# Optimization experiments

Hardware: AMD Instinct MI355X
Metric: run time of the kernel (lower is better)

The kernel has to match this reference:

```python
import jax, jax.numpy as jnp
import numpy as np

BIG_NUMBER = 1000000.0
B, N, H = 8, 256, 128   # batch, nodes, node/hidden feat
E, G = 128, 128         # edge feat, graph feat
MID, OUT = 128, 128
IN_Z = 2 * H


def setup_inputs() -> dict:
    key = jax.random.key(0)
    ks = jax.random.split(key, 20)
    sc = lambda fan_in: 1.0 / np.sqrt(fan_in)
    inp = {
        "node_fts": jax.random.normal(ks[0], (B, N, H), jnp.float32),
        "edge_fts": jax.random.normal(ks[1], (B, N, N, E), jnp.float32),
        "graph_fts": jax.random.normal(ks[2], (B, G), jnp.float32),
        "adj_mat": (jax.random.uniform(ks[3], (B, N, N)) < 0.5).astype(jnp.float32),
        "hidden": jax.random.normal(ks[4], (B, N, H), jnp.float32),
        # linear params, stored [in, out]
        "W1": jax.random.normal(ks[5], (IN_Z, MID), jnp.float32) * sc(IN_Z),
        "b1": jnp.zeros((MID,), jnp.float32),
        "W2": jax.random.normal(ks[6], (IN_Z, MID), jnp.float32) * sc(IN_Z),
        "b2": jnp.zeros((MID,), jnp.float32),
        "We": jax.random.normal(ks[7], (E, MID), jnp.float32) * sc(E),
        "be": jnp.zeros((MID,), jnp.float32),
        "Wg": jax.random.normal(ks[8], (G, MID), jnp.float32) * sc(G),
        "bg": jnp.zeros((MID,), jnp.float32),
        "Wo1": jax.random.normal(ks[9], (IN_Z, OUT), jnp.float32) * sc(IN_Z),
        "bo1": jnp.zeros((OUT,), jnp.float32),
        "Wo2": jax.random.normal(ks[10], (MID, OUT), jnp.float32) * sc(MID),
        "bo2": jnp.zeros((OUT,), jnp.float32),
    }
    return inp


def reference(node_fts, edge_fts, graph_fts, adj_mat, hidden,
              W1, b1, W2, b2, We, be, Wg, bg, Wo1, bo1, Wo2, bo2):
    # z: [b, n, 2h]
    z = jnp.concatenate([node_fts, hidden], axis=-1)
    msg_1 = z @ W1 + b1                       # [b, n, mid]
    msg_2 = z @ W2 + b2                       # [b, n, mid]
    msg_e = edge_fts @ We + be                # [b, n, n, mid]
    msg_g = graph_fts @ Wg + bg               # [b, mid]
    # msgs[b, i, j, :]; reduce over i (senders)
    msgs = (msg_1[:, None, :, :] + msg_2[:, :, None, :]
            + msg_e + msg_g[:, None, None, :])
    maxarg = jnp.where(adj_mat[..., None] > 0, msgs, -BIG_NUMBER)
    msgs_red = jnp.max(maxarg, axis=1)        # [b, n, mid]
    ret = jax.nn.relu((z @ Wo1 + bo1) + (msgs_red @ Wo2 + bo2))
    return ret
```

## Files before the change

kernel.cpp:

```cpp
#include <hip/hip_runtime.h>
#include <hip/hip_bf16.h>
#include <stdint.h>
#include <stddef.h>

#define B_   8
#define N_   256
#define H_   128
#define E_   128
#define INZ  256
#define BIGN 1000000.0f

typedef float f32x4 __attribute__((ext_vector_type(4)));
typedef short bf16x8 __attribute__((ext_vector_type(8)));

static __device__ __forceinline__ unsigned cvt2(float a, float b) {
    unsigned short ra = __builtin_bit_cast(unsigned short, __float2bfloat16(a));
    unsigned short rb = __builtin_bit_cast(unsigned short, __float2bfloat16(b));
    return (unsigned)ra | ((unsigned)rb << 16);
}

static __device__ __forceinline__ bf16x8 mk_frag(f32x4 lo, f32x4 h4) {
    union { unsigned u[4]; bf16x8 v; } r;
    r.u[0] = cvt2(lo.x, lo.y);
    r.u[1] = cvt2(lo.z, lo.w);
    r.u[2] = cvt2(h4.x, h4.y);
    r.u[3] = cvt2(h4.z, h4.w);
    return r.v;
}

#define GL16(gp, lp) __builtin_amdgcn_global_load_lds(                        \
    (const __attribute__((address_space(1))) unsigned int*)(gp),              \
    (__attribute__((address_space(3))) unsigned int*)(lp), 16, 0, 0)

__global__ __launch_bounds__(256) void prep_kernel(
    const float* __restrict__ node, const float* __restrict__ hidden,
    const float* __restrict__ gf,
    const float* __restrict__ W1, const float* __restrict__ b1,
    const float* __restrict__ W2, const float* __restrict__ b2,
    const float* __restrict__ Wg, const float* __restrict__ bg,
    const float* __restrict__ Wo1, const float* __restrict__ bo1,
    const float* __restrict__ We,
    float* __restrict__ msg1, float* __restrict__ m2g,
    float* __restrict__ zo1, unsigned short* __restrict__ weT)
{
    __shared__ float zs[4][INZ];
    const int t  = threadIdx.x;
    const int r0 = blockIdx.x * 4;
    const int b  = r0 >> 8;

    for (int idx = t; idx < 4 * INZ; idx += 256) {
        int r = idx >> 8, k = idx & 255;
        int row = r0 + r;
        zs[r][k] = (k < H_) ? node[(size_t)row * H_ + k]
                            : hidden[(size_t)row * H_ + (k - H_)];
    }
    if (blockIdx.x < 8) {
        int e0 = blockIdx.x * 2048;
        for (int e = e0 + t; e < e0 + 2048; e += 256) {
            int n = e >> 7, k = e & 127;
            weT[(n * 128 + k) ^ ((n & 7) << 3)] =
                (unsigned short)__builtin_bit_cast(unsigned short,
                    __float2bfloat16(We[k * 128 + n]));
        }
    }
    __syncthreads();

    const int col = t & 127;
    const int rg  = t >> 7;
    float a1[2] = {0, 0}, a2[2] = {0, 0}, ao[2] = {0, 0};

#pragma unroll 4
    for (int k = 0; k < INZ; ++k) {
        float w1 = W1[k * 128 + col];
        float w2 = W2[k * 128 + col];
        float wo = Wo1[k * 128 + col];
#pragma unroll
        for (int rr = 0; rr < 2; ++rr) {
            float zv = zs[rg * 2 + rr][k];
            a1[rr] = fmaf(zv, w1, a1[rr]);
            a2[rr] = fmaf(zv, w2, a2[rr]);
            ao[rr] = fmaf(zv, wo, ao[rr]);
        }
    }
    float mg = bg[col];
#pragma unroll 4
    for (int g = 0; g < 128; ++g)
        mg = fmaf(gf[b * 128 + g], Wg[g * 128 + col], mg);

    const float bb1 = b1[col], bb2 = b2[col], bbo = bo1[col];
#pragma unroll
    for (int rr = 0; rr < 2; ++rr) {
        size_t row = (size_t)(r0 + rg * 2 + rr);
        msg1[row * 128 + col] = a1[rr] + bb1;
        m2g[row * 128 + col]  = a2[rr] + bb2 + mg;
        zo1[row * 128 + col]  = ao[rr] + bbo;
    }
}

__global__ __launch_bounds__(256, 3) void pgn_main(
    const float* __restrict__ edge, const float* __restrict__ adj,
    const float* __restrict__ m2g, const unsigned short* __restrict__ weT,
    float* __restrict__ redp, int nsplit)
{
    __shared__ __align__(16) char smem[49152];

    const int t    = threadIdx.x;
    const int lane = t & 63, wid = t >> 6;
    const int wr   = wid >> 1, wn = wid & 1;
    const int hi   = lane >> 4, c15 = lane & 15;
    const int blk  = blockIdx.x;
    const int ih   = blk % nsplit;
    const int jblk = blk / nsplit;
    const int b    = jblk >> 6, jt = jblk & 63;
    const int j0   = jt * 4;
    const int irange = N_ / nsplit;
    const int ibase  = ih * irange;
    const int nt     = irange >> 3;

    bf16x8 bfr[4][4];
#pragma unroll
    for (int n = 0; n < 4; ++n) {
        int col = wn * 64 + n * 16 + c15;
        int sw  = (col & 7) << 3;
#pragma unroll
        for (int ks = 0; ks < 4; ++ks) {
            int sidx = (col * 128 + ks * 32 + hi * 8) ^ sw;
            bfr[n][ks] = *(const bf16x8*)(weT + sidx);
        }
    }

    const int l2 = lane >> 5;
    const int wb = (lane & 31) * 16;
    const char* gq0; const char* gq1; const char* gq2; const char* gq3;
    {
        const char* eb = (const char*)edge;
#pragma unroll
        for (int q = 0; q < 4; ++q) {
            int tr = wid * 8 + 2 * q + l2;
            int il = tr >> 2, jj = tr & 3;
            int sb = wb ^ ((tr & 7) << 4);
            const char* g = eb +
                (((size_t)(b * N_) + ibase + il) * N_ + (j0 + jj)) * 512 + sb;
            if (q == 0) gq0 = g; else if (q == 1) gq1 = g;
            else if (q == 2) gq2 = g; else gq3 = g;
        }
    }
    const unsigned woff = (unsigned)__builtin_amdgcn_readfirstlane(wid * 4096);

    char* pa = smem;
    char* pb = smem + 16384;
    char* pc = smem + 32768;

    GL16(gq0, pa + woff);
    GL16(gq1, pa + woff + 1024);
    GL16(gq2, pa + woff + 2048);
    GL16(gq3, pa + woff + 3072);

    const int trc = wr * 16 + c15;
    const unsigned abase = (unsigned)((trc * 512 + hi * 32) ^ ((trc & 7) << 4));
    const int il_l = wr * 4 + hi;

    float rmax[4][4];
#pragma unroll
    for (int n = 0; n < 4; ++n)
#pragma unroll
        for (int rg = 0; rg < 4; ++rg) rmax[n][rg] = -BIGN;

    for (int it = 0; it < nt; ++it) {
        const int ig = ibase + it * 8 + il_l;
        f32x4 a4 = *(const f32x4*)(adj + (size_t)(b * N_ + ig) * N_ + j0);
        const float* mp = m2g + (size_t)(b * N_ + ig) * 128 + wn * 64 + c15;
        float mv0 = mp[0], mv1 = mp[16], mv2 = mp[32], mv3 = mp[48];

        if (it + 1 < nt) {
            size_t toff = (size_t)(it + 1) * (8u * N_ * E_ * 4u);
            GL16(gq0 + toff, pb + woff);
            GL16(gq1 + toff, pb + woff + 1024);
            GL16(gq2 + toff, pb + woff + 2048);
            GL16(gq3 + toff, pb + woff + 3072);
            asm volatile("s_waitcnt vmcnt(9)" ::: "memory");
        } else {
            asm volatile("s_waitcnt vmcnt(5)" ::: "memory");
        }
        __builtin_amdgcn_s_barrier();
        __builtin_amdgcn_sched_barrier(0);

        f32x4 acc[4] = {};
#pragma unroll
        for (int ks = 0; ks < 4; ++ks) {
            f32x4 lo = *(const f32x4*)(pa + (abase + ks * 128));
            f32x4 h4 = *(const f32x4*)(pa + ((abase ^ 16) + ks * 128));
            bf16x8 af = mk_frag(lo, h4);
#pragma unroll
            for (int n = 0; n < 4; ++n)
                acc[n] = __builtin_amdgcn_mfma_f32_16x16x32_bf16(
                    af, bfr[n][ks], acc[n], 0, 0, 0);
        }

        float mvs[4] = {mv0, mv1, mv2, mv3};
#pragma unroll
        for (int n = 0; n < 4; ++n)
#pragma unroll
            for (int rg = 0; rg < 4; ++rg) {
                float v = acc[n][rg] + mvs[n];
                v = (a4[rg] > 0.0f) ? v : -BIGN;
                rmax[n][rg] = fmaxf(rmax[n][rg], v);
            }

        char* tp = pa; pa = pb; pb = pc; pc = tp;
    }

#pragma unroll
    for (int n = 0; n < 4; ++n)
#pragma unroll
        for (int rg = 0; rg < 4; ++rg) {
            float v = rmax[n][rg];
            v = fmaxf(v, __shfl_xor(v, 16, 64));
            v = fmaxf(v, __shfl_xor(v, 32, 64));
            rmax[n][rg] = v;
        }
    __syncthreads();
    float* redb = (float*)smem;
    if (wr == 0 && lane < 16) {
#pragma unroll
        for (int n = 0; n < 4; ++n)
#pragma unroll
            for (int rg = 0; rg < 4; ++rg)
                redb[rg * 128 + wn * 64 + n * 16 + c15] = rmax[n][rg];
    }
    __syncthreads();
    if (wr == 1 && lane < 16) {
#pragma unroll
        for (int n = 0; n < 4; ++n)
#pragma unroll
            for (int rg = 0; rg < 4; ++rg) {
                int e = rg * 128 + wn * 64 + n * 16 + c15;
                redb[e] = fmaxf(redb[e], rmax[n][rg]);
            }
    }
    __syncthreads();
    for (int e = t; e < 512; e += 256)
        redp[(size_t)blk * 512 + e] = redb[e];
}

__global__ __launch_bounds__(256) void finish_kernel(
    const float* __restrict__ redp, const float* __restrict__ msg1,
    const float* __restrict__ zo1, const float* __restrict__ be,
    const float* __restrict__ Wo2, const float* __restrict__ bo2,
    float* __restrict__ out, int nsplit)
{
    __shared__ float rb[8][128];
    const int t  = threadIdx.x;
    const int r0 = blockIdx.x * 8;

    for (int idx = t; idx < 1024; idx += 256) {
        int rr = idx >> 7, k = idx & 127;
        int r = r0 + rr;
        int jblk = r >> 2, jj = r & 3;
        float v = -BIGN - 1.0f;
        for (int p = 0; p < nsplit; ++p)
            v = fmaxf(v, redp[(size_t)(jblk * nsplit + p) * 512 + jj * 128 + k]);
        rb[rr][k] = v + msg1[(size_t)r * 128 + k] + be[k];
    }
    __syncthreads();

    const int col = t & 127;
    const int half = t >> 7;
#pragma unroll
    for (int rx = 0; rx < 4; ++rx) {
        int rr = half * 4 + rx;
        size_t row = (size_t)(r0 + rr);
        float a = 0.0f;
#pragma unroll 8
        for (int k = 0; k < 128; ++k)
            a = fmaf(rb[rr][k], Wo2[k * 128 + col], a);
        float o = zo1[row * 128 + col] + bo2[col] + a;
        out[row * 128 + col] = fmaxf(o, 0.0f);
    }
}

extern "C" void kernel_launch(void* const* d_in, const int* in_sizes, int n_in,
                              void* d_out, int out_size, void* d_ws, size_t ws_size,
                              hipStream_t stream) {
    const float* node   = (const float*)d_in[0];
    const float* edge   = (const float*)d_in[1];
    const float* gf     = (const float*)d_in[2];
    const float* adj    = (const float*)d_in[3];
    const float* hidden = (const float*)d_in[4];
    const float* W1  = (const float*)d_in[5];
    const float* b1  = (const float*)d_in[6];
    const float* W2  = (const float*)d_in[7];
    const float* b2  = (const float*)d_in[8];
    const float* We  = (const float*)d_in[9];
    const float* be  = (const float*)d_in[10];
    const float* Wg  = (const float*)d_in[11];
    const float* bg  = (const float*)d_in[12];
    const float* Wo1 = (const float*)d_in[13];
    const float* bo1 = (const float*)d_in[14];
    const float* Wo2 = (const float*)d_in[15];
    const float* bo2 = (const float*)d_in[16];
    float* out = (float*)d_out;

    float* msg1 = (float*)d_ws;
    float* m2g  = msg1 + 2048 * 128;
    float* zo1  = m2g + 2048 * 128;
    unsigned short* weT = (unsigned short*)(zo1 + 2048 * 128);
    float* redp = (float*)((char*)weT + 128 * 128 * sizeof(unsigned short));

    const size_t base_bytes = 3u * 1048576u + 32768u;
    int nsplit = (ws_size >= base_bytes + 2u * 1048576u) ? 2 : 1;

    hipLaunchKernelGGL(prep_kernel, dim3(512), dim3(256), 0, stream,
                       node, hidden, gf, W1, b1, W2, b2, Wg, bg, Wo1, bo1, We,
                       msg1, m2g, zo1, weT);
    hipLaunchKernelGGL(pgn_main, dim3(512 * nsplit), dim3(256), 0, stream,
                       edge, adj, m2g, weT, redp, nsplit);
    hipLaunchKernelGGL(finish_kernel, dim3(256), dim3(256), 0, stream,
                       redp, msg1, zo1, be, Wo2, bo2, out, nsplit);
}
```

Measured before the change: 106.2 us.

## Replace LDS-staged edge pipeline with direct global loads and wide per-wave tiles

The main kernel no longer stages edge tiles through shared memory with async global-to-LDS copies, triple buffering and barriers. Each wave now reads its edge rows straight from global memory into registers and computes all 128 output columns using 8 MFMA column tiles. The grid is reorganised so each block covers 16 senders and 64 receivers. Cross-block partial maxima are written as full 64x128 tiles and reduced over 16 sender chunks in the finish kernel. The aim is to remove LDS traffic and synchronisation. The cost is a much larger partial-result workspace (extra write and read traffic), less explicit load overlap, and possibly overrunning the workspace size the old code checked for.

Measured after the change: 120.3 us. 1.13x slower.

```diff
diff --git a/kernel.cpp b/kernel.cpp
--- a/kernel.cpp
+++ b/kernel.cpp
@@ -27,10 +27,6 @@
     r.u[3] = cvt2(h4.z, h4.w);
     return r.v;
 }
-
-#define GL16(gp, lp) __builtin_amdgcn_global_load_lds(                        \
-    (const __attribute__((address_space(1))) unsigned int*)(gp),              \
-    (__attribute__((address_space(3))) unsigned int*)(lp), 16, 0, 0)
 
 __global__ __launch_bounds__(256) void prep_kernel(
     const float* __restrict__ node, const float* __restrict__ hidden,
@@ -58,9 +54,8 @@
         int e0 = blockIdx.x * 2048;
         for (int e = e0 + t; e < e0 + 2048; e += 256) {
             int n = e >> 7, k = e & 127;
-            weT[(n * 128 + k) ^ ((n & 7) << 3)] =
-                (unsigned short)__builtin_bit_cast(unsigned short,
-                    __float2bfloat16(We[k * 128 + n]));
+            weT[e] = (unsigned short)__builtin_bit_cast(unsigned short,
+                         __float2bfloat16(We[k * 128 + n]));
         }
     }
     __syncthreads();
@@ -97,157 +92,85 @@
     }
 }
 
-__global__ __launch_bounds__(256, 3) void pgn_main(
+__global__ __launch_bounds__(256, 2) void pgn_main(
     const float* __restrict__ edge, const float* __restrict__ adj,
     const float* __restrict__ m2g, const unsigned short* __restrict__ weT,
-    float* __restrict__ redp, int nsplit)
+    float* __restrict__ redp)
 {
-    __shared__ __align__(16) char smem[49152];
-
     const int t    = threadIdx.x;
     const int lane = t & 63, wid = t >> 6;
-    const int wr   = wid >> 1, wn = wid & 1;
     const int hi   = lane >> 4, c15 = lane & 15;
     const int blk  = blockIdx.x;
-    const int ih   = blk % nsplit;
-    const int jblk = blk / nsplit;
-    const int b    = jblk >> 6, jt = jblk & 63;
-    const int j0   = jt * 4;
-    const int irange = N_ / nsplit;
-    const int ibase  = ih * irange;
-    const int nt     = irange >> 3;
-
-    bf16x8 bfr[4][4];
-#pragma unroll
-    for (int n = 0; n < 4; ++n) {
-        int col = wn * 64 + n * 16 + c15;
-        int sw  = (col & 7) << 3;
+    const int b    = blk >> 6;
+    const int ic   = (blk >> 2) & 15;
+    const int jq   = blk & 3;
+    const int i0   = ic * 16;
+    const int jrow = jq * 64 + wid * 16 + c15;
+
+    bf16x8 bfr[8][4];
+#pragma unroll
+    for (int n = 0; n < 8; ++n) {
+#pragma unroll
+        for (int ks = 0; ks < 4; ++ks)
+            bfr[n][ks] = *(const bf16x8*)(weT + (n * 16 + c15) * 128 + ks * 32 + hi * 8);
+    }
+
+    float rmax[8][4];
+#pragma unroll
+    for (int n = 0; n < 8; ++n)
+#pragma unroll
+        for (int rg = 0; rg < 4; ++rg) rmax[n][rg] = -BIGN;
+
+    const float* abase = edge + ((size_t)(b * N_ + i0) * N_ + jrow) * E_ + hi * 8;
+    const float* adjb  = adj + (size_t)(b * N_ + i0) * N_ + jq * 64 + wid * 16 + hi * 4;
+    const float* m2gb  = m2g + (size_t)(b * N_ + i0) * 128 + c15;
+
+#pragma unroll 2
+    for (int ii = 0; ii < 16; ++ii) {
+        const float* ar = abase + (size_t)ii * (N_ * E_);
+
+        f32x4 a4 = *(const f32x4*)(adjb + (size_t)ii * N_);
+        float mv[8];
+#pragma unroll
+        for (int n = 0; n < 8; ++n) mv[n] = m2gb[(size_t)ii * 128 + n * 16];
+
+        f32x4 acc[8] = {};
 #pragma unroll
         for (int ks = 0; ks < 4; ++ks) {
-            int sidx = (col * 128 + ks * 32 + hi * 8) ^ sw;
-            bfr[n][ks] = *(const bf16x8*)(weT + sidx);
-        }
-    }
-
-    const int l2 = lane >> 5;
-    const int wb = (lane & 31) * 16;
-    const char* gq0; const char* gq1; const char* gq2; const char* gq3;
-    {
-        const char* eb = (const char*)edge;
-#pragma unroll
-        for (int q = 0; q < 4; ++q) {
-            int tr = wid * 8 + 2 * q + l2;
-            int il = tr >> 2, jj = tr & 3;
-            int sb = wb ^ ((tr & 7) << 4);
-            const char* g = eb +
-                (((size_t)(b * N_) + ibase + il) * N_ + (j0 + jj)) * 512 + sb;
-            if (q == 0) gq0 = g; else if (q == 1) gq1 = g;
-            else if (q == 2) gq2 = g; else gq3 = g;
-        }
-    }
-    const unsigned woff = (unsigned)__builtin_amdgcn_readfirstlane(wid * 4096);
-
-    char* pa = smem;
-    char* pb = smem + 16384;
-    char* pc = smem + 32768;
-
-    GL16(gq0, pa + woff);
-    GL16(gq1, pa + woff + 1024);
-    GL16(gq2, pa + woff + 2048);
-    GL16(gq3, pa + woff + 3072);
-
-    const int trc = wr * 16 + c15;
-    const unsigned abase = (unsigned)((trc * 512 + hi * 32) ^ ((trc & 7) << 4));
-    const int il_l = wr * 4 + hi;
-
-    float rmax[4][4];
-#pragma unroll
-    for (int n = 0; n < 4; ++n)
-#pragma unroll
-        for (int rg = 0; rg < 4; ++rg) rmax[n][rg] = -BIGN;
-
-    for (int it = 0; it < nt; ++it) {
-        const int ig = ibase + it * 8 + il_l;
-        f32x4 a4 = *(const f32x4*)(adj + (size_t)(b * N_ + ig) * N_ + j0);
-        const float* mp = m2g + (size_t)(b * N_ + ig) * 128 + wn * 64 + c15;
-        float mv0 = mp[0], mv1 = mp[16], mv2 = mp[32], mv3 = mp[48];
-
-        if (it + 1 < nt) {
-            size_t toff = (size_t)(it + 1) * (8u * N_ * E_ * 4u);
-            GL16(gq0 + toff, pb + woff);
-            GL16(gq1 + toff, pb + woff + 1024);
-            GL16(gq2 + toff, pb + woff + 2048);
-            GL16(gq3 + toff, pb + woff + 3072);
-            asm volatile("s_waitcnt vmcnt(9)" ::: "memory");
-        } else {
-            asm volatile("s_waitcnt vmcnt(5)" ::: "memory");
-        }
-        __builtin_amdgcn_s_barrier();
-        __builtin_amdgcn_sched_barrier(0);
-
-        f32x4 acc[4] = {};
-#pragma unroll
-        for (int ks = 0; ks < 4; ++ks) {
-            f32x4 lo = *(const f32x4*)(pa + (abase + ks * 128));
-            f32x4 h4 = *(const f32x4*)(pa + ((abase ^ 16) + ks * 128));
+            f32x4 lo = *(const f32x4*)(ar + ks * 32);
+            f32x4 h4 = *(const f32x4*)(ar + ks * 32 + 4);
             bf16x8 af = mk_frag(lo, h4);
 #pragma unroll
-            for (int n = 0; n < 4; ++n)
+            for (int n = 0; n < 8; ++n)
                 acc[n] = __builtin_amdgcn_mfma_f32_16x16x32_bf16(
                     af, bfr[n][ks], acc[n], 0, 0, 0);
         }
 
-        float mvs[4] = {mv0, mv1, mv2, mv3};
-#pragma unroll
-        for (int n = 0; n < 4; ++n)
+#pragma unroll
+        for (int n = 0; n < 8; ++n)
 #pragma unroll
             for (int rg = 0; rg < 4; ++rg) {
-                float v = acc[n][rg] + mvs[n];
+                float v = acc[n][rg] + mv[n];
                 v = (a4[rg] > 0.0f) ? v : -BIGN;
                 rmax[n][rg] = fmaxf(rmax[n][rg], v);
             }
-
-        char* tp = pa; pa = pb; pb = pc; pc = tp;
-    }
-
-#pragma unroll
-    for (int n = 0; n < 4; ++n)
+    }
+
+    float* rp = redp + (size_t)blk * 8192;
+#pragma unroll
+    for (int n = 0; n < 8; ++n)
 #pragma unroll
         for (int rg = 0; rg < 4; ++rg) {
-            float v = rmax[n][rg];
-            v = fmaxf(v, __shfl_xor(v, 16, 64));
-            v = fmaxf(v, __shfl_xor(v, 32, 64));
-            rmax[n][rg] = v;
-        }
-    __syncthreads();
-    float* redb = (float*)smem;
-    if (wr == 0 && lane < 16) {
-#pragma unroll
-        for (int n = 0; n < 4; ++n)
-#pragma unroll
-            for (int rg = 0; rg < 4; ++rg)
-                redb[rg * 128 + wn * 64 + n * 16 + c15] = rmax[n][rg];
-    }
-    __syncthreads();
-    if (wr == 1 && lane < 16) {
-#pragma unroll
-        for (int n = 0; n < 4; ++n)
-#pragma unroll
-            for (int rg = 0; rg < 4; ++rg) {
-                int e = rg * 128 + wn * 64 + n * 16 + c15;
-                redb[e] = fmaxf(redb[e], rmax[n][rg]);
-            }
-    }
-    __syncthreads();
-    for (int e = t; e < 512; e += 256)
-        redp[(size_t)blk * 512 + e] = redb[e];
+            int jl = wid * 16 + hi * 4 + rg;
+            rp[jl * 128 + n * 16 + c15] = rmax[n][rg];
+        }
 }
 
 __global__ __launch_bounds__(256) void finish_kernel(
     const float* __restrict__ redp, const float* __restrict__ msg1,
     const float* __restrict__ zo1, const float* __restrict__ be,
     const float* __restrict__ Wo2, const float* __restrict__ bo2,
-    float* __restrict__ out, int nsplit)
+    float* __restrict__ out)
 {
     __shared__ float rb[8][128];
     const int t  = threadIdx.x;
@@ -255,16 +178,18 @@
 
     for (int idx = t; idx < 1024; idx += 256) {
         int rr = idx >> 7, k = idx & 127;
-        int r = r0 + rr;
-        int jblk = r >> 2, jj = r & 3;
+        int r  = r0 + rr;
+        int b  = r >> 8, j = r & 255;
+        int jq = j >> 6, jl = j & 63;
         float v = -BIGN - 1.0f;
-        for (int p = 0; p < nsplit; ++p)
-            v = fmaxf(v, redp[(size_t)(jblk * nsplit + p) * 512 + jj * 128 + k]);
+#pragma unroll 4
+        for (int ic = 0; ic < 16; ++ic)
+            v = fmaxf(v, redp[(size_t)(((b * 16 + ic) * 4) + jq) * 8192 + jl * 128 + k]);
         rb[rr][k] = v + msg1[(size_t)r * 128 + k] + be[k];
     }
     __syncthreads();
 
-    const int col = t & 127;
+    const int col  = t & 127;
     const int half = t >> 7;
 #pragma unroll
     for (int rx = 0; rx < 4; ++rx) {
@@ -307,14 +232,11 @@
     unsigned short* weT = (unsigned short*)(zo1 + 2048 * 128);
     float* redp = (float*)((char*)weT + 128 * 128 * sizeof(unsigned short));
 
-    const size_t base_bytes = 3u * 1048576u + 32768u;
-    int nsplit = (ws_size >= base_bytes + 2u * 1048576u) ? 2 : 1;
-
     hipLaunchKernelGGL(prep_kernel, dim3(512), dim3(256), 0, stream,
                        node, hidden, gf, W1, b1, W2, b2, Wg, bg, Wo1, bo1, We,
                        msg1, m2g, zo1, weT);
-    hipLaunchKernelGGL(pgn_main, dim3(512 * nsplit), dim3(256), 0, stream,
-                       edge, adj, m2g, weT, redp, nsplit);
+    hipLaunchKernelGGL(pgn_main, dim3(512), dim3(256), 0, stream,
+                       edge, adj, m2g, weT, redp);
     hipLaunchKernelGGL(finish_kernel, dim3(256), dim3(256), 0, stream,
-                       redp, msg1, zo1, be, Wo2, bo2, out, nsplit);
-}
+                       redp, msg1, zo1, be, Wo2, bo2, out);
+}
```
